# Optimization experiments

Measured on AMD Instinct MI355X. Metric: run time of the kernel, lower is better.

Reference implementation:

```python
import jax, jax.numpy as jnp
import numpy as np
import math

D_MODEL = 768
NUM_HEADS = 12
D_K = D_MODEL // NUM_HEADS
B, S = 4, 2048


def setup_inputs() -> dict:
    key = jax.random.key(0)
    ks = jax.random.split(key, 11)
    s = 1.0 / math.sqrt(D_MODEL)
    inp = {
        "q": jax.random.normal(ks[0], (B, S, D_MODEL), jnp.float32),
        "k": jax.random.normal(ks[1], (B, S, D_MODEL), jnp.float32),
        "v": jax.random.normal(ks[2], (B, S, D_MODEL), jnp.float32),
        "w_q": jax.random.normal(ks[3], (D_MODEL, D_MODEL), jnp.float32) * s,
        "b_q": jax.random.normal(ks[4], (D_MODEL,), jnp.float32) * s,
        "w_k": jax.random.normal(ks[5], (D_MODEL, D_MODEL), jnp.float32) * s,
        "b_k": jax.random.normal(ks[6], (D_MODEL,), jnp.float32) * s,
        "w_v": jax.random.normal(ks[7], (D_MODEL, D_MODEL), jnp.float32) * s,
        "b_v": jax.random.normal(ks[8], (D_MODEL,), jnp.float32) * s,
        "w_o": jax.random.normal(ks[9], (D_MODEL, D_MODEL), jnp.float32) * s,
        "b_o": jax.random.normal(ks[10], (D_MODEL,), jnp.float32) * s,
    }
    return inp


def reference(q, k, v, w_q, b_q, w_k, b_k, w_v, b_v, w_o, b_o):
    b = q.shape[0]
    # Linear projections (torch Linear: x @ W.T + b), reshape to [B,H,S,d_k]
    def proj(x, w, bias):
        y = x @ w.T + bias
        return y.reshape(b, -1, NUM_HEADS, D_K).transpose(0, 2, 1, 3)

    qh = proj(q, w_q, b_q)
    kh = proj(k, w_k, b_k)
    vh = proj(v, w_v, b_v)

    scale = 1.0 / math.sqrt(D_K)
    scores = jnp.einsum("bhqd,bhkd->bhqk", qh, kh) * scale  # [B,H,S,S]
    attn = jax.nn.softmax(scores, axis=-1)
    # dropout is identity in eval mode
    out = jnp.einsum("bhqk,bhkd->bhqd", attn, vh)
    out = out.transpose(0, 2, 1, 3).reshape(b, -1, D_MODEL)
    return out @ w_o.T + b_o
```

## Files before the change

### kernel.cpp

```cpp
#include <hip/hip_runtime.h>

#define DEV __device__ __forceinline__

typedef __attribute__((ext_vector_type(8))) short short8;
typedef __attribute__((ext_vector_type(4))) float f32x4;
typedef unsigned short u16;
typedef unsigned int u32;

DEV f32x4 mfma16(short8 a, short8 b, f32x4 c) {
    return __builtin_amdgcn_mfma_f32_16x16x32_bf16(a, b, c, 0, 0, 0);
}

DEV u16 f2bf(float f) {
    unsigned u = __builtin_bit_cast(unsigned, f);
    u += 0x7fffu + ((u >> 16) & 1u);
    return (u16)(u >> 16);
}

DEV u32 cvt_pk_bf16(float a, float b) {
    u32 r;
    asm("v_cvt_pk_bf16_f32 %0, %1, %2" : "=v"(r) : "v"(a), "v"(b));
    return r;
}

DEV float fexp2_scaled(float xs) {
    int i = (int)xs + 1065055420;
    return __builtin_bit_cast(float, i);
}

DEV void gload16(const void* g, const void* l) {
    __builtin_amdgcn_global_load_lds(
        (const __attribute__((address_space(1))) unsigned int*)g,
        (__attribute__((address_space(3))) unsigned int*)l, 16, 0, 0);
}

template<int N> DEV void waitvm_barrier() {
    asm volatile("s_waitcnt vmcnt(%0)\n\ts_barrier" :: "n"(N) : "memory");
}

DEV short8 lds_frag_swz(const u16* base, int row, int chunk) {
    int sc = chunk ^ (row & 7);
    return *(const short8*)((const char*)base + row * 128 + sc * 16);
}

__global__ __launch_bounds__(256) void prep(
    const float* __restrict__ q, const float* __restrict__ k, const float* __restrict__ v,
    const float* __restrict__ wq, const float* __restrict__ wk,
    const float* __restrict__ wv, const float* __restrict__ wo,
    u16* __restrict__ xq, u16* __restrict__ xk, u16* __restrict__ xv,
    u16* __restrict__ wqB, u16* __restrict__ wkB, u16* __restrict__ wvB,
    u16* __restrict__ woB)
{
    int b = blockIdx.x;
    const float* s;
    u16* d;
    int i;
    if (b < 18432) {
        int t = b / 6144, r = b % 6144;
        s = t == 0 ? q : t == 1 ? k : v;
        d = t == 0 ? xq : t == 1 ? xk : xv;
        i = r * 256 + threadIdx.x;
    } else {
        int t = (b - 18432) / 576, r = (b - 18432) % 576;
        s = t == 0 ? wq : t == 1 ? wk : t == 2 ? wv : wo;
        d = t == 0 ? wqB : t == 1 ? wkB : t == 2 ? wvB : woB;
        i = r * 256 + threadIdx.x;
    }
    float4 vv = ((const float4*)s)[i];
    ((ushort4*)d)[i] = make_ushort4(f2bf(vv.x), f2bf(vv.y), f2bf(vv.z), f2bf(vv.w));
}

template<int MODE>
DEV void gemm_bf16_body(const u16* __restrict__ A_g, const u16* __restrict__ B_g,
                        const float* __restrict__ bias, float scale,
                        u16* __restrict__ outP, float* __restrict__ outF,
                        int mBase, int nBase)
{
    __shared__ u16 AS[128 * 64], BS[128 * 64];

    const int tid = threadIdx.x;
    const int l = tid & 63, wid = tid >> 6;
    const int wy = wid >> 1, wx = wid & 1;
    const int lr = l & 15, lg = l >> 4;

    f32x4 acc[4][4];
    for (int i = 0; i < 4; ++i)
        for (int j = 0; j < 4; ++j) acc[i][j] = (f32x4)0.0f;

    for (int kt = 0; kt < 12; ++kt) {
        if (kt) __syncthreads();
        for (int r = 0; r < 4; ++r) {
            int c = tid + r * 256;
            int row = c >> 3;
            int sc = (c & 7) ^ (row & 7);
            size_t gA = (size_t)(mBase + row) * 768 + kt * 64 + sc * 8;
            size_t gB = (size_t)(nBase + row) * 768 + kt * 64 + sc * 8;
            gload16(A_g + gA, AS + (size_t)(r * 256 + wid * 64) * 8);
            gload16(B_g + gB, BS + (size_t)(r * 256 + wid * 64) * 8);
        }
        __syncthreads();

        short8 bf[4][2];
        for (int nt = 0; nt < 4; ++nt)
            for (int ks = 0; ks < 2; ++ks)
                bf[nt][ks] = lds_frag_swz(BS, wx * 64 + nt * 16 + lr, ks * 4 + lg);
        for (int mt = 0; mt < 4; ++mt) {
            short8 ah[2];
            for (int ks = 0; ks < 2; ++ks)
                ah[ks] = lds_frag_swz(AS, wy * 64 + mt * 16 + lr, ks * 4 + lg);
            for (int nt = 0; nt < 4; ++nt)
                for (int ks = 0; ks < 2; ++ks)
                    acc[mt][nt] = mfma16(ah[ks], bf[nt][ks], acc[mt][nt]);
        }
    }

    for (int mt = 0; mt < 4; ++mt)
        for (int nt = 0; nt < 4; ++nt) {
            int colg = nBase + wx * 64 + nt * 16 + lr;
            for (int r = 0; r < 4; ++r) {
                int rowg = mBase + wy * 64 + mt * 16 + lg * 4 + r;
                float bv = (MODE == 2) ? bias[rowg] : bias[colg];
                float vv = (acc[mt][nt][r] + bv) * scale;
                if constexpr (MODE == 0) {
                    int b = rowg >> 11, s = rowg & 2047;
                    int h = colg >> 6, d = colg & 63;
                    outP[((size_t)(b * 12 + h) * 2048 + s) * 64 + d] = f2bf(vv);
                } else if constexpr (MODE == 1) {
                    outF[(size_t)rowg * 768 + colg] = vv;
                } else {
                    int b = colg >> 11, s = colg & 2047;
                    int h = rowg >> 6, d = rowg & 63;
                    outP[((size_t)(b * 12 + h) * 64 + d) * 2048 + s] = f2bf(vv);
                }
            }
        }
}

__global__ __launch_bounds__(256, 4) void gemm_proj(
    const u16* __restrict__ xq, const u16* __restrict__ xk, const u16* __restrict__ xv,
    const u16* __restrict__ wq, const u16* __restrict__ wk, const u16* __restrict__ wv,
    const float* __restrict__ bq, const float* __restrict__ bk, const float* __restrict__ bv,
    u16* __restrict__ Qpl, u16* __restrict__ Kpl, u16* __restrict__ Vtp)
{
    int z = blockIdx.z;
    if (z < 2) {
        const u16* X = z ? xk : xq;
        const u16* W = z ? wk : wq;
        const float* bias = z ? bk : bq;
        float scale = z ? 1.0f : 0.125f * 1.44269504f * 8388608.0f;
        u16* o = z ? Kpl : Qpl;
        gemm_bf16_body<0>(X, W, bias, scale, o, nullptr, blockIdx.y * 128, blockIdx.x * 128);
    } else {
        gemm_bf16_body<2>(wv, xv, bv, 1.0f, Vtp, nullptr, blockIdx.x * 128, blockIdx.y * 128);
    }
}

__global__ __launch_bounds__(256, 4) void gemm_out(
    const u16* __restrict__ Op, const u16* __restrict__ woB,
    const float* __restrict__ bias, float* __restrict__ outF)
{
    gemm_bf16_body<1>(Op, woB, bias, 1.0f, nullptr, outF,
                      blockIdx.y * 128, blockIdx.x * 128);
}

__global__ __launch_bounds__(256, 3) void attn4(
    const u16* __restrict__ Qp, const u16* __restrict__ Kp,
    const u16* __restrict__ Vtp, u16* __restrict__ Op)
{
    __shared__ u16 Ks[2][64 * 64], Vs[2][64 * 64];
    __shared__ u16 Eh[128][72];

    const int tid = threadIdx.x;
    const int l = tid & 63, wid = tid >> 6;
    const int lr = l & 15, lg = l >> 4;
    const int bh = blockIdx.x, qt = blockIdx.y;

    short8 q_h[2][2];
    for (int s = 0; s < 2; ++s) {
        size_t qrow = ((size_t)bh * 2048 + qt * 128 + wid * 32 + s * 16 + lr) * 64;
        q_h[s][0] = *(const short8*)(Qp + qrow + lg * 8);
        q_h[s][1] = *(const short8*)(Qp + qrow + 32 + lg * 8);
    }

    short8 ones;
    for (int j = 0; j < 8; ++j) ones[j] = (short)0x3F80;

    f32x4 num[2][4];
    for (int s = 0; s < 2; ++s)
        for (int nt = 0; nt < 4; ++nt) num[s][nt] = (f32x4)0.0f;
    f32x4 denacc[2] = {(f32x4)0.0f, (f32x4)0.0f};

    auto stageK = [&](int kb, int p) {
        for (int r = 0; r < 2; ++r) {
            int c = tid + r * 256;
            int row = c >> 3, sc = (c & 7) ^ (row & 7);
            size_t g = ((size_t)bh * 2048 + kb * 64 + row) * 64 + sc * 8;
            gload16(Kp + g, Ks[p] + (size_t)(r * 256 + wid * 64) * 8);
        }
    };
    auto stageV = [&](int kb, int p) {
        for (int r = 0; r < 2; ++r) {
            int c = tid + r * 256;
            int row = c >> 3, sc = (c & 7) ^ (row & 7);
            size_t g = ((size_t)bh * 64 + row) * 2048 + kb * 64 + sc * 8;
            gload16(Vtp + g, Vs[p] + (size_t)(r * 256 + wid * 64) * 8);
        }
    };

    stageK(0, 0);
    stageV(0, 0);

    for (int kb = 0; kb < 32; ++kb) {
        const int p = kb & 1;
        waitvm_barrier<0>();
        if (kb < 31) {
            stageK(kb + 1, p ^ 1);
            stageV(kb + 1, p ^ 1);
        }

        f32x4 st[2][4];
        for (int s = 0; s < 2; ++s)
            for (int nt = 0; nt < 4; ++nt) st[s][nt] = (f32x4)0.0f;
        __builtin_amdgcn_s_setprio(1);
        for (int nt = 0; nt < 4; ++nt)
            for (int ks = 0; ks < 2; ++ks) {
                short8 kh = lds_frag_swz(Ks[p], nt * 16 + lr, ks * 4 + lg);
                st[0][nt] = mfma16(kh, q_h[0][ks], st[0][nt]);
                st[1][nt] = mfma16(kh, q_h[1][ks], st[1][nt]);
            }
        __builtin_amdgcn_s_setprio(0);

        for (int s = 0; s < 2; ++s)
            for (int nt = 0; nt < 4; ++nt) {
                u32 pk0 = cvt_pk_bf16(fexp2_scaled(st[s][nt][0]), fexp2_scaled(st[s][nt][1]));
                u32 pk1 = cvt_pk_bf16(fexp2_scaled(st[s][nt][2]), fexp2_scaled(st[s][nt][3]));
                int erow = wid * 32 + s * 16 + lr;
                *(u32*)&Eh[erow][nt * 16 + lg * 4]     = pk0;
                *(u32*)&Eh[erow][nt * 16 + lg * 4 + 2] = pk1;
            }

        short8 e[2][2];
        for (int s = 0; s < 2; ++s) {
            int erow = wid * 32 + s * 16 + lr;
            e[s][0] = *(const short8*)&Eh[erow][lg * 8];
            e[s][1] = *(const short8*)&Eh[erow][32 + lg * 8];
        }
        __builtin_amdgcn_s_setprio(1);
        denacc[0] = mfma16(e[0][0], ones, denacc[0]);
        denacc[0] = mfma16(e[0][1], ones, denacc[0]);
        denacc[1] = mfma16(e[1][0], ones, denacc[1]);
        denacc[1] = mfma16(e[1][1], ones, denacc[1]);
        for (int nt = 0; nt < 4; ++nt)
            for (int ks = 0; ks < 2; ++ks) {
                short8 vh = lds_frag_swz(Vs[p], nt * 16 + lr, ks * 4 + lg);
                num[0][nt] = mfma16(e[0][ks], vh, num[0][nt]);
                num[1][nt] = mfma16(e[1][ks], vh, num[1][nt]);
            }
        __builtin_amdgcn_s_setprio(0);
    }

    const int b = bh / 12, h = bh % 12;
    for (int s = 0; s < 2; ++s) {
        float rden[4];
        for (int r = 0; r < 4; ++r) rden[r] = 1.0f / denacc[s][r];
        for (int nt = 0; nt < 4; ++nt)
            for (int r = 0; r < 4; ++r) {
                int srow = qt * 128 + wid * 32 + s * 16 + lg * 4 + r;
                size_t rowg = (size_t)b * 2048 + srow;
                int col = h * 64 + nt * 16 + lr;
                Op[rowg * 768 + col] = f2bf(num[s][nt][r] * rden[r]);
            }
    }
}

extern "C" void kernel_launch(void* const* d_in, const int* in_sizes, int n_in,
                              void* d_out, int out_size, void* d_ws, size_t ws_size,
                              hipStream_t stream)
{
    const float* q   = (const float*)d_in[0];
    const float* k   = (const float*)d_in[1];
    const float* v   = (const float*)d_in[2];
    const float* w_q = (const float*)d_in[3];
    const float* b_q = (const float*)d_in[4];
    const float* w_k = (const float*)d_in[5];
    const float* b_k = (const float*)d_in[6];
    const float* w_v = (const float*)d_in[7];
    const float* b_v = (const float*)d_in[8];
    const float* w_o = (const float*)d_in[9];
    const float* b_o = (const float*)d_in[10];
    float* out = (float*)d_out;

    const size_t PL  = (size_t)48 * 2048 * 64;
    const size_t WPL = (size_t)768 * 768;
    u16* base = (u16*)d_ws;
    u16* xqB = base;
    u16* xkB = base + PL;
    u16* xvB = base + 2 * PL;
    u16* Qpl = base + 3 * PL;
    u16* Kpl = base + 4 * PL;
    u16* Vtp = base + 5 * PL;
    u16* OP  = base + 6 * PL;
    u16* W   = base + 7 * PL;
    u16* wqB = W;
    u16* wkB = W + WPL;
    u16* wvB = W + 2 * WPL;
    u16* woB = W + 3 * WPL;

    dim3 bt(256, 1, 1);
    hipLaunchKernelGGL(prep, dim3(20736), bt, 0, stream,
                       q, k, v, w_q, w_k, w_v, w_o,
                       xqB, xkB, xvB, wqB, wkB, wvB, woB);

    hipLaunchKernelGGL(gemm_proj, dim3(6, 64, 3), bt, 0, stream,
                       xqB, xkB, xvB, wqB, wkB, wvB, b_q, b_k, b_v,
                       Qpl, Kpl, Vtp);

    hipLaunchKernelGGL(attn4, dim3(48, 16), bt, 0, stream,
                       Qpl, Kpl, Vtp, OP);

    hipLaunchKernelGGL(gemm_out, dim3(6, 64), bt, 0, stream,
                       OP, woB, b_o, out);
}
```

Measured before the change: 156.0 us.

## Fuse fp32-to-bf16 input conversion into projection GEMM and shrink attention KV tile

The projection GEMM now reads the fp32 q/k/v activations directly, converts them to bf16 in registers and writes them into swizzled LDS. The prep kernel then only converts the weights, which removes a full write and re-read of three bf16 activation copies. Separately, the attention kernel's K/V block shrinks from 64 to 32 keys, which halves LDS per block and raises the occupancy hint from 3 to 6. The trade-offs are that the fused A/B loads use synchronous register loads instead of async global-to-LDS copies, and attention runs twice as many loop iterations and barriers.

```diff
diff --git a/kernel.cpp b/kernel.cpp
--- a/kernel.cpp
+++ b/kernel.cpp
@@ -42,39 +42,32 @@
     int sc = chunk ^ (row & 7);
     return *(const short8*)((const char*)base + row * 128 + sc * 16);
 }
+DEV short8 lds_frag_swz32(const u16* base, int row, int chunk) {
+    int sc = chunk ^ (row & 3);
+    return *(const short8*)((const char*)base + row * 64 + sc * 16);
+}
 
 __global__ __launch_bounds__(256) void prep(
-    const float* __restrict__ q, const float* __restrict__ k, const float* __restrict__ v,
     const float* __restrict__ wq, const float* __restrict__ wk,
     const float* __restrict__ wv, const float* __restrict__ wo,
-    u16* __restrict__ xq, u16* __restrict__ xk, u16* __restrict__ xv,
     u16* __restrict__ wqB, u16* __restrict__ wkB, u16* __restrict__ wvB,
     u16* __restrict__ woB)
 {
     int b = blockIdx.x;
-    const float* s;
-    u16* d;
-    int i;
-    if (b < 18432) {
-        int t = b / 6144, r = b % 6144;
-        s = t == 0 ? q : t == 1 ? k : v;
-        d = t == 0 ? xq : t == 1 ? xk : xv;
-        i = r * 256 + threadIdx.x;
-    } else {
-        int t = (b - 18432) / 576, r = (b - 18432) % 576;
-        s = t == 0 ? wq : t == 1 ? wk : t == 2 ? wv : wo;
-        d = t == 0 ? wqB : t == 1 ? wkB : t == 2 ? wvB : woB;
-        i = r * 256 + threadIdx.x;
-    }
+    int t = b / 576, r = b % 576;
+    const float* s = t == 0 ? wq : t == 1 ? wk : t == 2 ? wv : wo;
+    u16* d = t == 0 ? wqB : t == 1 ? wkB : t == 2 ? wvB : woB;
+    int i = r * 256 + threadIdx.x;
     float4 vv = ((const float4*)s)[i];
     ((ushort4*)d)[i] = make_ushort4(f2bf(vv.x), f2bf(vv.y), f2bf(vv.z), f2bf(vv.w));
 }
 
-template<int MODE>
-DEV void gemm_bf16_body(const u16* __restrict__ A_g, const u16* __restrict__ B_g,
-                        const float* __restrict__ bias, float scale,
-                        u16* __restrict__ outP, float* __restrict__ outF,
-                        int mBase, int nBase)
+template<int AF32, int BF32, int MODE>
+DEV void gemm_body(const float* __restrict__ Af, const u16* __restrict__ A_g,
+                   const float* __restrict__ Bf, const u16* __restrict__ B_g,
+                   const float* __restrict__ bias, float scale,
+                   u16* __restrict__ outP, float* __restrict__ outF,
+                   int mBase, int nBase)
 {
     __shared__ u16 AS[128 * 64], BS[128 * 64];
 
@@ -89,14 +82,43 @@
 
     for (int kt = 0; kt < 12; ++kt) {
         if (kt) __syncthreads();
-        for (int r = 0; r < 4; ++r) {
-            int c = tid + r * 256;
-            int row = c >> 3;
-            int sc = (c & 7) ^ (row & 7);
-            size_t gA = (size_t)(mBase + row) * 768 + kt * 64 + sc * 8;
-            size_t gB = (size_t)(nBase + row) * 768 + kt * 64 + sc * 8;
-            gload16(A_g + gA, AS + (size_t)(r * 256 + wid * 64) * 8);
-            gload16(B_g + gB, BS + (size_t)(r * 256 + wid * 64) * 8);
+        if constexpr (AF32) {
+            for (int i = 0; i < 8; ++i) {
+                int f = tid + i * 256;
+                int row = f >> 4, q4 = f & 15;
+                float4 xv = *(const float4*)(Af + (size_t)(mBase + row) * 768 + kt * 64 + q4 * 4);
+                u32 lo = cvt_pk_bf16(xv.x, xv.y);
+                u32 hi = cvt_pk_bf16(xv.z, xv.w);
+                int byteOff = row * 128 + (((q4 >> 1) ^ (row & 7)) * 16) + (q4 & 1) * 8;
+                *(uint2*)((char*)AS + byteOff) = make_uint2(lo, hi);
+            }
+        } else {
+            for (int r = 0; r < 4; ++r) {
+                int c = tid + r * 256;
+                int row = c >> 3;
+                int sc = (c & 7) ^ (row & 7);
+                size_t g = (size_t)(mBase + row) * 768 + kt * 64 + sc * 8;
+                gload16(A_g + g, AS + (size_t)(r * 256 + wid * 64) * 8);
+            }
+        }
+        if constexpr (BF32) {
+            for (int i = 0; i < 8; ++i) {
+                int f = tid + i * 256;
+                int row = f >> 4, q4 = f & 15;
+                float4 xv = *(const float4*)(Bf + (size_t)(nBase + row) * 768 + kt * 64 + q4 * 4);
+                u32 lo = cvt_pk_bf16(xv.x, xv.y);
+                u32 hi = cvt_pk_bf16(xv.z, xv.w);
+                int byteOff = row * 128 + (((q4 >> 1) ^ (row & 7)) * 16) + (q4 & 1) * 8;
+                *(uint2*)((char*)BS + byteOff) = make_uint2(lo, hi);
+            }
+        } else {
+            for (int r = 0; r < 4; ++r) {
+                int c = tid + r * 256;
+                int row = c >> 3;
+                int sc = (c & 7) ^ (row & 7);
+                size_t g = (size_t)(nBase + row) * 768 + kt * 64 + sc * 8;
+                gload16(B_g + g, BS + (size_t)(r * 256 + wid * 64) * 8);
+            }
         }
         __syncthreads();
 
@@ -137,21 +159,22 @@
 }
 
 __global__ __launch_bounds__(256, 4) void gemm_proj(
-    const u16* __restrict__ xq, const u16* __restrict__ xk, const u16* __restrict__ xv,
-    const u16* __restrict__ wq, const u16* __restrict__ wk, const u16* __restrict__ wv,
+    const float* __restrict__ q, const float* __restrict__ k, const float* __restrict__ v,
+    const u16* __restrict__ wqB, const u16* __restrict__ wkB, const u16* __restrict__ wvB,
     const float* __restrict__ bq, const float* __restrict__ bk, const float* __restrict__ bv,
     u16* __restrict__ Qpl, u16* __restrict__ Kpl, u16* __restrict__ Vtp)
 {
     int z = blockIdx.z;
-    if (z < 2) {
-        const u16* X = z ? xk : xq;
-        const u16* W = z ? wk : wq;
-        const float* bias = z ? bk : bq;
-        float scale = z ? 1.0f : 0.125f * 1.44269504f * 8388608.0f;
-        u16* o = z ? Kpl : Qpl;
-        gemm_bf16_body<0>(X, W, bias, scale, o, nullptr, blockIdx.y * 128, blockIdx.x * 128);
+    if (z == 0) {
+        gemm_body<1, 0, 0>(q, nullptr, nullptr, wqB, bq,
+                           0.125f * 1.44269504f * 8388608.0f, Qpl, nullptr,
+                           blockIdx.y * 128, blockIdx.x * 128);
+    } else if (z == 1) {
+        gemm_body<1, 0, 0>(k, nullptr, nullptr, wkB, bk, 1.0f, Kpl, nullptr,
+                           blockIdx.y * 128, blockIdx.x * 128);
     } else {
-        gemm_bf16_body<2>(wv, xv, bv, 1.0f, Vtp, nullptr, blockIdx.x * 128, blockIdx.y * 128);
+        gemm_body<0, 1, 2>(nullptr, wvB, v, nullptr, bv, 1.0f, Vtp, nullptr,
+                           blockIdx.x * 128, blockIdx.y * 128);
     }
 }
 
@@ -159,16 +182,16 @@
     const u16* __restrict__ Op, const u16* __restrict__ woB,
     const float* __restrict__ bias, float* __restrict__ outF)
 {
-    gemm_bf16_body<1>(Op, woB, bias, 1.0f, nullptr, outF,
-                      blockIdx.y * 128, blockIdx.x * 128);
-}
-
-__global__ __launch_bounds__(256, 3) void attn4(
+    gemm_body<0, 0, 1>(nullptr, Op, nullptr, woB, bias, 1.0f, nullptr, outF,
+                       blockIdx.y * 128, blockIdx.x * 128);
+}
+
+__global__ __launch_bounds__(256, 6) void attn4(
     const u16* __restrict__ Qp, const u16* __restrict__ Kp,
     const u16* __restrict__ Vtp, u16* __restrict__ Op)
 {
-    __shared__ u16 Ks[2][64 * 64], Vs[2][64 * 64];
-    __shared__ u16 Eh[128][72];
+    __shared__ u16 Ks[2][32 * 64], Vs[2][64 * 32];
+    __shared__ u16 Eh[128][40];
 
     const int tid = threadIdx.x;
     const int l = tid & 63, wid = tid >> 6;
@@ -191,38 +214,32 @@
     f32x4 denacc[2] = {(f32x4)0.0f, (f32x4)0.0f};
 
     auto stageK = [&](int kb, int p) {
-        for (int r = 0; r < 2; ++r) {
-            int c = tid + r * 256;
-            int row = c >> 3, sc = (c & 7) ^ (row & 7);
-            size_t g = ((size_t)bh * 2048 + kb * 64 + row) * 64 + sc * 8;
-            gload16(Kp + g, Ks[p] + (size_t)(r * 256 + wid * 64) * 8);
-        }
+        int row = tid >> 3, sc = (tid & 7) ^ (row & 7);
+        size_t g = ((size_t)bh * 2048 + kb * 32 + row) * 64 + sc * 8;
+        gload16(Kp + g, Ks[p] + (size_t)wid * 512);
     };
     auto stageV = [&](int kb, int p) {
-        for (int r = 0; r < 2; ++r) {
-            int c = tid + r * 256;
-            int row = c >> 3, sc = (c & 7) ^ (row & 7);
-            size_t g = ((size_t)bh * 64 + row) * 2048 + kb * 64 + sc * 8;
-            gload16(Vtp + g, Vs[p] + (size_t)(r * 256 + wid * 64) * 8);
-        }
+        int row = tid >> 2, sc = (tid & 3) ^ (row & 3);
+        size_t g = ((size_t)bh * 64 + row) * 2048 + kb * 32 + sc * 8;
+        gload16(Vtp + g, Vs[p] + (size_t)wid * 512);
     };
 
     stageK(0, 0);
     stageV(0, 0);
 
-    for (int kb = 0; kb < 32; ++kb) {
+    for (int kb = 0; kb < 64; ++kb) {
         const int p = kb & 1;
         waitvm_barrier<0>();
-        if (kb < 31) {
+        if (kb < 63) {
             stageK(kb + 1, p ^ 1);
             stageV(kb + 1, p ^ 1);
         }
 
-        f32x4 st[2][4];
+        f32x4 st[2][2];
         for (int s = 0; s < 2; ++s)
-            for (int nt = 0; nt < 4; ++nt) st[s][nt] = (f32x4)0.0f;
+            for (int nt = 0; nt < 2; ++nt) st[s][nt] = (f32x4)0.0f;
         __builtin_amdgcn_s_setprio(1);
-        for (int nt = 0; nt < 4; ++nt)
+        for (int nt = 0; nt < 2; ++nt)
             for (int ks = 0; ks < 2; ++ks) {
                 short8 kh = lds_frag_swz(Ks[p], nt * 16 + lr, ks * 4 + lg);
                 st[0][nt] = mfma16(kh, q_h[0][ks], st[0][nt]);
@@ -231,7 +248,7 @@
         __builtin_amdgcn_s_setprio(0);
 
         for (int s = 0; s < 2; ++s)
-            for (int nt = 0; nt < 4; ++nt) {
+            for (int nt = 0; nt < 2; ++nt) {
                 u32 pk0 = cvt_pk_bf16(fexp2_scaled(st[s][nt][0]), fexp2_scaled(st[s][nt][1]));
                 u32 pk1 = cvt_pk_bf16(fexp2_scaled(st[s][nt][2]), fexp2_scaled(st[s][nt][3]));
                 int erow = wid * 32 + s * 16 + lr;
@@ -239,23 +256,16 @@
                 *(u32*)&Eh[erow][nt * 16 + lg * 4 + 2] = pk1;
             }
 
-        short8 e[2][2];
-        for (int s = 0; s < 2; ++s) {
-            int erow = wid * 32 + s * 16 + lr;
-            e[s][0] = *(const short8*)&Eh[erow][lg * 8];
-            e[s][1] = *(const short8*)&Eh[erow][32 + lg * 8];
-        }
+        short8 e0 = *(const short8*)&Eh[wid * 32 + lr][lg * 8];
+        short8 e1 = *(const short8*)&Eh[wid * 32 + 16 + lr][lg * 8];
         __builtin_amdgcn_s_setprio(1);
-        denacc[0] = mfma16(e[0][0], ones, denacc[0]);
-        denacc[0] = mfma16(e[0][1], ones, denacc[0]);
-        denacc[1] = mfma16(e[1][0], ones, denacc[1]);
-        denacc[1] = mfma16(e[1][1], ones, denacc[1]);
-        for (int nt = 0; nt < 4; ++nt)
-            for (int ks = 0; ks < 2; ++ks) {
-                short8 vh = lds_frag_swz(Vs[p], nt * 16 + lr, ks * 4 + lg);
-                num[0][nt] = mfma16(e[0][ks], vh, num[0][nt]);
-                num[1][nt] = mfma16(e[1][ks], vh, num[1][nt]);
-            }
+        denacc[0] = mfma16(e0, ones, denacc[0]);
+        denacc[1] = mfma16(e1, ones, denacc[1]);
+        for (int nt = 0; nt < 4; ++nt) {
+            short8 vh = lds_frag_swz32(Vs[p], nt * 16 + lr, lg);
+            num[0][nt] = mfma16(e0, vh, num[0][nt]);
+            num[1][nt] = mfma16(e1, vh, num[1][nt]);
+        }
         __builtin_amdgcn_s_setprio(0);
     }
 
@@ -293,26 +303,22 @@
     const size_t PL  = (size_t)48 * 2048 * 64;
     const size_t WPL = (size_t)768 * 768;
     u16* base = (u16*)d_ws;
-    u16* xqB = base;
-    u16* xkB = base + PL;
-    u16* xvB = base + 2 * PL;
-    u16* Qpl = base + 3 * PL;
-    u16* Kpl = base + 4 * PL;
-    u16* Vtp = base + 5 * PL;
-    u16* OP  = base + 6 * PL;
-    u16* W   = base + 7 * PL;
+    u16* Qpl = base;
+    u16* Kpl = base + PL;
+    u16* Vtp = base + 2 * PL;
+    u16* OP  = base + 3 * PL;
+    u16* W   = base + 4 * PL;
     u16* wqB = W;
     u16* wkB = W + WPL;
     u16* wvB = W + 2 * WPL;
     u16* woB = W + 3 * WPL;
 
     dim3 bt(256, 1, 1);
-    hipLaunchKernelGGL(prep, dim3(20736), bt, 0, stream,
-                       q, k, v, w_q, w_k, w_v, w_o,
-                       xqB, xkB, xvB, wqB, wkB, wvB, woB);
+    hipLaunchKernelGGL(prep, dim3(2304), bt, 0, stream,
+                       w_q, w_k, w_v, w_o, wqB, wkB, wvB, woB);
 
     hipLaunchKernelGGL(gemm_proj, dim3(6, 64, 3), bt, 0, stream,
-                       xqB, xkB, xvB, wqB, wkB, wvB, b_q, b_k, b_v,
+                       q, k, v, wqB, wkB, wvB, b_q, b_k, b_v,
                        Qpl, Kpl, Vtp);
 
     hipLaunchKernelGGL(attn4, dim3(48, 16), bt, 0, stream,
```

New measurement: 257.2 us. +64.9%, slower.
